# Kernel tuning notes

Hardware: AMD Instinct MI355X
Metric: run time of the kernel (lower is better)

The kernel has to match this reference:

```python
import jax, jax.numpy as jnp
import numpy as np

BATCH = 8192
IN_CH = 64          # input_channels
CH = 256            # output channels per row
BOARD = 27          # board_edge**3
EDGE = 3
ROWS = 49           # 3*(board_edge+1)**2 + 1


def _wincon_mats():
    # Faithful port of init_wincon_matrix(); returns (27, 3, 49) 0/1 matrix.
    step = [0]
    mats = np.zeros((BOARD, EDGE, ROWS), dtype=np.float32)
    col = 0
    x = y = z = 0

    def put():
        mats[x + 3 * y + 9 * z, step[0], col] = 1
        step[0] = (step[0] + 1) % 3

    for x in range(3):
        for y in range(3):
            for z in range(3):
                put()
            col += 1
        for z in range(3):
            for y in range(3):
                put()
            col += 1
        for y in range(3):
            z = y
            put()
        col += 1
        for y in range(3):
            z = 2 - y
            put()
        col += 1
    for z in range(3):
        for y in range(3):
            for x in range(3):
                put()
            col += 1
        for y in range(3):
            x = y
            put()
        col += 1
        for y in range(3):
            x = 2 - y
            put()
        col += 1
    for y in range(3):
        for z in range(3):
            x = z
            put()
        col += 1
        for z in range(3):
            x = 2 - z
            put()
        col += 1
    for x in range(3):
        y = z = x
        put()
    col += 1
    for x in range(3):
        y = z = 2 - x
        put()
    col += 1
    for x in range(3):
        y = x
        z = 2 - x
        put()
    col += 1
    for x in range(3):
        z = x
        y = 2 - x
        put()
    col += 1
    return mats


_MATS = jnp.asarray(_wincon_mats())  # (board_size=27, edge=3, row_count=49)


def setup_inputs() -> dict:
    key = jax.random.key(0)
    k1, k2, k3 = jax.random.split(key, 3)
    x = jax.random.normal(k1, (BATCH, IN_CH * BOARD), dtype=jnp.float32)
    # keras 'random_normal' initializer: stddev 0.05
    v = jax.random.normal(k2, (EDGE, IN_CH, ROWS, CH), dtype=jnp.float32) * 0.05
    b = jax.random.normal(k3, (CH * ROWS,), dtype=jnp.float32) * 0.05
    return {"x": x, "v": v, "b": b}


def reference(x, v, b):
    # Weight synthesis: w[bd, i, r, c] = sum_e mats[bd, e, r] * v[e, i, r, c]
    # (same math as the broadcast+multiply+reduce in the original, fused via einsum)
    w = jnp.einsum('ber,eirc->birc', _MATS, v)            # (27, in_ch, 49, ch)
    w = w.reshape(BOARD * IN_CH, ROWS * CH)              # (1728, 12544)
    return x @ w + b
```

## Files before the change

### kernel.cpp

```cpp
#include <hip/hip_runtime.h>
#include <cstdint>
#include <cstddef>


#define XCOLS   1728
#define ROWS_W  49
#define KTOT    192
#define OUTW    12544

typedef __attribute__((ext_vector_type(8))) short short8;
typedef __attribute__((ext_vector_type(4))) float f32x4;

struct CellTab { int c[ROWS_W][3]; };

constexpr CellTab make_cells() {
    CellTab t{};
    int step = 0, col = 0;
    int x = 0, y = 0, z = 0;
#define PUT() do { t.c[col][step] = x + 3*y + 9*z; step = (step + 1) % 3; } while (0)
    for (x = 0; x < 3; ++x) {
        for (y = 0; y < 3; ++y) {
            for (z = 0; z < 3; ++z) PUT();
            ++col;
        }
        for (z = 0; z < 3; ++z) {
            for (y = 0; y < 3; ++y) PUT();
            ++col;
        }
        for (y = 0; y < 3; ++y) { z = y; PUT(); }
        ++col;
        for (y = 0; y < 3; ++y) { z = 2 - y; PUT(); }
        ++col;
    }
    for (z = 0; z < 3; ++z) {
        for (y = 0; y < 3; ++y) {
            for (x = 0; x < 3; ++x) PUT();
            ++col;
        }
        for (y = 0; y < 3; ++y) { x = y; PUT(); }
        ++col;
        for (y = 0; y < 3; ++y) { x = 2 - y; PUT(); }
        ++col;
    }
    for (y = 0; y < 3; ++y) {
        for (z = 0; z < 3; ++z) { x = z; PUT(); }
        ++col;
        for (z = 0; z < 3; ++z) { x = 2 - z; PUT(); }
        ++col;
    }
    for (x = 0; x < 3; ++x) { y = x; z = x; PUT(); }
    ++col;
    for (x = 0; x < 3; ++x) { y = 2 - x; z = 2 - x; PUT(); }
    ++col;
    for (x = 0; x < 3; ++x) { y = x; z = 2 - x; PUT(); }
    ++col;
    for (x = 0; x < 3; ++x) { z = x; y = 2 - x; PUT(); }
    ++col;
#undef PUT
    return t;
}

__constant__ CellTab CELLS = make_cells();

__device__ __forceinline__ unsigned short f2bf(float f) {
    union { float f; unsigned u; } a; a.f = f;
    unsigned u = a.u;
    return (unsigned short)((u + 0x7fffu + ((u >> 16) & 1u)) >> 16);
}

__global__ __launch_bounds__(256) void wt_prepass(const float* __restrict__ v,
                                                  unsigned short* __restrict__ wt) {
    const int kc = blockIdx.x;
    const int r  = blockIdx.y;
    const int c  = threadIdx.x;
#pragma unroll
    for (int q = 0; q < 4; ++q) {
        short8 s;
#pragma unroll
        for (int j = 0; j < 8; ++j) {
            const int k = kc * 32 + q * 8 + j;
            s[j] = (short)f2bf(v[(size_t)k * OUTW + r * 256 + c]);
        }
        *(short8*)(wt + ((((size_t)r * 6 + kc) * 4 + q) * 256 + c) * 8) = s;
    }
}

__global__ __launch_bounds__(256, 2) void tic_gemm(
    const float* __restrict__ x,
    const unsigned short* __restrict__ wt,
    const float* __restrict__ bias,
    float* __restrict__ out)
{
    const int swz = (blockIdx.x & 7) * 392 + (blockIdx.x >> 3);
    const int m     = swz / 49;
    const int r     = swz % 49;
    const int mbase = m * 128;

    const int t    = threadIdx.x;
    const int wave = t >> 6;
    const int lane = t & 63;
    const int l15  = lane & 15;
    const int quad = lane >> 4;
    const int half = wave & 1;
    const int wh   = wave >> 1;

    const int cells[3] = { CELLS.c[r][0], CELLS.c[r][1], CELLS.c[r][2] };

    f32x4 acc[4][8];
#pragma unroll
    for (int nt = 0; nt < 8; ++nt) {
        const float bv = bias[r * 256 + half * 128 + nt * 16 + l15];
        f32x4 a; a[0] = bv; a[1] = bv; a[2] = bv; a[3] = bv;
#pragma unroll
        for (int mt = 0; mt < 4; ++mt) acc[mt][nt] = a;
    }

    const unsigned short* wbase =
        wt + ((size_t)(r * 24 + quad) * 256 + half * 128 + l15) * 8;

    short8 afr[2][4];
    short8 bfr[2][8];

    auto loadA = [&](int kc, int p) {
        const int e = kc >> 1, h = kc & 1;
        const int colb = cells[e] * 64 + h * 32 + quad * 8;
#pragma unroll
        for (int mt = 0; mt < 4; ++mt) {
            const int row = mbase + wh * 64 + mt * 16 + l15;
            const float* src = x + (size_t)row * XCOLS + colb;
            const float4 a0 = *(const float4*)src;
            const float4 a1 = *(const float4*)(src + 4);
            short8 s;
            s[0] = (short)f2bf(a0.x); s[1] = (short)f2bf(a0.y);
            s[2] = (short)f2bf(a0.z); s[3] = (short)f2bf(a0.w);
            s[4] = (short)f2bf(a1.x); s[5] = (short)f2bf(a1.y);
            s[6] = (short)f2bf(a1.z); s[7] = (short)f2bf(a1.w);
            afr[p][mt] = s;
        }
    };
    auto loadB = [&](int kc, int p) {
        const unsigned short* src = wbase + (size_t)kc * 8192;
#pragma unroll
        for (int nt = 0; nt < 8; ++nt)
            bfr[p][nt] = *(const short8*)(src + nt * 128);
    };

    loadA(0, 0);
    loadB(0, 0);

#pragma unroll
    for (int kc = 0; kc < 6; ++kc) {
        const int p = kc & 1;
        if (kc < 5) {
            loadB(kc + 1, p ^ 1);
            loadA(kc + 1, p ^ 1);
        }
#pragma unroll
        for (int nt = 0; nt < 8; ++nt) {
#pragma unroll
            for (int mt = 0; mt < 4; ++mt)
                acc[mt][nt] = __builtin_amdgcn_mfma_f32_16x16x32_bf16(
                    afr[p][mt], bfr[p][nt], acc[mt][nt], 0, 0, 0);
        }
    }

#pragma unroll
    for (int mt = 0; mt < 4; ++mt) {
#pragma unroll
        for (int v4 = 0; v4 < 4; ++v4) {
            const int row = mbase + wh * 64 + mt * 16 + quad * 4 + v4;
            float* orow = out + (size_t)row * OUTW + r * 256 + half * 128;
#pragma unroll
            for (int nt = 0; nt < 8; ++nt)
                __builtin_nontemporal_store(acc[mt][nt][v4], orow + nt * 16 + l15);
        }
    }
}

extern "C" void kernel_launch(void* const* d_in, const int* in_sizes, int n_in,
                              void* d_out, int out_size, void* d_ws, size_t ws_size,
                              hipStream_t stream) {
    const float* x  = (const float*)d_in[0];
    const float* v  = (const float*)d_in[1];
    const float* b  = (const float*)d_in[2];
    float* out = (float*)d_out;

    unsigned short* wt = (unsigned short*)d_ws;

    wt_prepass<<<dim3(6, 49), dim3(256), 0, stream>>>(v, wt);
    tic_gemm<<<dim3(64 * 49), dim3(256), 0, stream>>>(x, wt, b, out);
}
```

Measured before the change: 533.3 us.

## Stage 32-row x tile in LDS as bf16 and loop over all 49 rows per block

Each block now loads a 32-row slice of x once, converts it to bf16 into XOR-swizzled shared memory, and then loops over all 49 output row groups, reading A fragments from LDS. This removes the repeated global reads and bf16 conversion of x, which were previously done 49 times per row tile. The trade-off is a much smaller grid of 256 blocks with about 110KB of LDS each, so occupancy is one block per CU. The per-row loop is not unrolled, so loads of B from global memory are exposed and there is less tiling per wave.

Result: no change. 529.6 us (-0.7%).

```diff
diff --git a/kernel.cpp b/kernel.cpp
--- a/kernel.cpp
+++ b/kernel.cpp
@@ -9,6 +9,7 @@
 #define OUTW    12544
 
 typedef __attribute__((ext_vector_type(8))) short short8;
+typedef __attribute__((ext_vector_type(4))) short short4v;
 typedef __attribute__((ext_vector_type(4))) float f32x4;
 
 struct CellTab { int c[ROWS_W][3]; };
@@ -85,94 +86,99 @@
     }
 }
 
-__global__ __launch_bounds__(256, 2) void tic_gemm(
+__global__ __launch_bounds__(256) void tic_gemm(
     const float* __restrict__ x,
     const unsigned short* __restrict__ wt,
     const float* __restrict__ bias,
     float* __restrict__ out)
 {
-    const int swz = (blockIdx.x & 7) * 392 + (blockIdx.x >> 3);
-    const int m     = swz / 49;
-    const int r     = swz % 49;
-    const int mbase = m * 128;
-
+    const int mbase = blockIdx.x * 32;
     const int t    = threadIdx.x;
     const int wave = t >> 6;
     const int lane = t & 63;
     const int l15  = lane & 15;
     const int quad = lane >> 4;
-    const int half = wave & 1;
-    const int wh   = wave >> 1;
 
-    const int cells[3] = { CELLS.c[r][0], CELLS.c[r][1], CELLS.c[r][2] };
+    __shared__ __align__(16) unsigned short Xs[32 * 216 * 8];
 
-    f32x4 acc[4][8];
-#pragma unroll
-    for (int nt = 0; nt < 8; ++nt) {
-        const float bv = bias[r * 256 + half * 128 + nt * 16 + l15];
-        f32x4 a; a[0] = bv; a[1] = bv; a[2] = bv; a[3] = bv;
-#pragma unroll
-        for (int mt = 0; mt < 4; ++mt) acc[mt][nt] = a;
+#pragma unroll 6
+    for (int i = 0; i < 54; ++i) {
+        const int flat = i * 256 + t;
+        const int row  = flat / 432;
+        const int c4   = flat - row * 432;
+        const float4 a = *(const float4*)(x + (size_t)(mbase + row) * XCOLS + c4 * 4);
+        const int c16 = c4 >> 1, hh = c4 & 1;
+        const int sc  = c16 ^ (row & 7);
+        short4v s;
+        s[0] = (short)f2bf(a.x); s[1] = (short)f2bf(a.y);
+        s[2] = (short)f2bf(a.z); s[3] = (short)f2bf(a.w);
+        *(short4v*)&Xs[(row * 216 + sc) * 8 + hh * 4] = s;
     }
+    __syncthreads();
 
-    const unsigned short* wbase =
-        wt + ((size_t)(r * 24 + quad) * 256 + half * 128 + l15) * 8;
+    f32x4  acc[2][4];
+    short8 afr[2][2];
+    short8 bfr[2][4];
 
-    short8 afr[2][4];
-    short8 bfr[2][8];
-
-    auto loadA = [&](int kc, int p) {
-        const int e = kc >> 1, h = kc & 1;
-        const int colb = cells[e] * 64 + h * 32 + quad * 8;
-#pragma unroll
-        for (int mt = 0; mt < 4; ++mt) {
-            const int row = mbase + wh * 64 + mt * 16 + l15;
-            const float* src = x + (size_t)row * XCOLS + colb;
-            const float4 a0 = *(const float4*)src;
-            const float4 a1 = *(const float4*)(src + 4);
-            short8 s;
-            s[0] = (short)f2bf(a0.x); s[1] = (short)f2bf(a0.y);
-            s[2] = (short)f2bf(a0.z); s[3] = (short)f2bf(a0.w);
-            s[4] = (short)f2bf(a1.x); s[5] = (short)f2bf(a1.y);
-            s[6] = (short)f2bf(a1.z); s[7] = (short)f2bf(a1.w);
-            afr[p][mt] = s;
-        }
-    };
-    auto loadB = [&](int kc, int p) {
-        const unsigned short* src = wbase + (size_t)kc * 8192;
-#pragma unroll
-        for (int nt = 0; nt < 8; ++nt)
-            bfr[p][nt] = *(const short8*)(src + nt * 128);
-    };
-
-    loadA(0, 0);
-    loadB(0, 0);
+#pragma unroll 1
+    for (int r = 0; r < ROWS_W; ++r) {
+        const int c0 = CELLS.c[r][0], c1 = CELLS.c[r][1], c2 = CELLS.c[r][2];
+        const int cell[3] = { c0, c1, c2 };
 
 #pragma unroll
-    for (int kc = 0; kc < 6; ++kc) {
-        const int p = kc & 1;
-        if (kc < 5) {
-            loadB(kc + 1, p ^ 1);
-            loadA(kc + 1, p ^ 1);
+        for (int nt = 0; nt < 4; ++nt) {
+            const float bv = bias[r * 256 + wave * 64 + nt * 16 + l15];
+            f32x4 a; a[0] = bv; a[1] = bv; a[2] = bv; a[3] = bv;
+            acc[0][nt] = a; acc[1][nt] = a;
         }
+
+        auto loadA = [&](int kc, int p) {
+            const int e = kc >> 1, h = kc & 1;
+            const int cb = cell[e] * 8 + h * 4 + quad;
 #pragma unroll
-        for (int nt = 0; nt < 8; ++nt) {
+            for (int mt = 0; mt < 2; ++mt) {
+                const int row = mt * 16 + l15;
+                afr[p][mt] = *(const short8*)&Xs[(row * 216 + (cb ^ (l15 & 7))) * 8];
+            }
+        };
+        auto loadB = [&](int kc, int p) {
+            const unsigned short* src =
+                wt + ((size_t)((r * 6 + kc) * 4 + quad) * 256 + wave * 64 + l15) * 8;
 #pragma unroll
-            for (int mt = 0; mt < 4; ++mt)
-                acc[mt][nt] = __builtin_amdgcn_mfma_f32_16x16x32_bf16(
-                    afr[p][mt], bfr[p][nt], acc[mt][nt], 0, 0, 0);
-        }
-    }
+            for (int nt = 0; nt < 4; ++nt)
+                bfr[p][nt] = *(const short8*)(src + nt * 128);
+        };
+
+        loadA(0, 0);
+        loadB(0, 0);
 
 #pragma unroll
-    for (int mt = 0; mt < 4; ++mt) {
+        for (int kc = 0; kc < 6; ++kc) {
+            const int p = kc & 1;
+            if (kc < 5) {
+                loadB(kc + 1, p ^ 1);
+                loadA(kc + 1, p ^ 1);
+            }
 #pragma unroll
-        for (int v4 = 0; v4 < 4; ++v4) {
-            const int row = mbase + wh * 64 + mt * 16 + quad * 4 + v4;
-            float* orow = out + (size_t)row * OUTW + r * 256 + half * 128;
+            for (int nt = 0; nt < 4; ++nt) {
 #pragma unroll
-            for (int nt = 0; nt < 8; ++nt)
-                __builtin_nontemporal_store(acc[mt][nt][v4], orow + nt * 16 + l15);
+                for (int mt = 0; mt < 2; ++mt)
+                    acc[mt][nt] = __builtin_amdgcn_mfma_f32_16x16x32_bf16(
+                        afr[p][mt], bfr[p][nt], acc[mt][nt], 0, 0, 0);
+            }
+        }
+
+#pragma unroll
+        for (int mt = 0; mt < 2; ++mt) {
+#pragma unroll
+            for (int v4 = 0; v4 < 4; ++v4) {
+                const int row = mbase + mt * 16 + quad * 4 + v4;
+                float* orow = out + (size_t)row * OUTW + r * 256 + wave * 64;
+#pragma unroll
+                for (int nt = 0; nt < 4; ++nt)
+                    __builtin_nontemporal_store(acc[mt][nt][v4],
+                                                orow + nt * 16 + l15);
+            }
         }
     }
 }
@@ -188,5 +194,5 @@
     unsigned short* wt = (unsigned short*)d_ws;
 
     wt_prepass<<<dim3(6, 49), dim3(256), 0, stream>>>(v, wt);
-    tic_gemm<<<dim3(64 * 49), dim3(256), 0, stream>>>(x, wt, b, out);
+    tic_gemm<<<dim3(8192 / 32), dim3(256), 0, stream>>>(x, wt, b, out);
 }
```
